# Kernel optimization log

Hardware: AMD Instinct MI355X
Metric: run time of the kernel (lower is better)

## Reference

```python
import jax, jax.numpy as jnp
import numpy as np

NUM_HEADS = 8
H_DIM = 24
COORDS_DIM = 3
NUM_W_PER_DIST = 8
BLOCK_SIZE = 128
N_HASHES = 3
N = 32768
HASH_DIM = H_DIM + (COORDS_DIM - 1) + 2  # q/k augmented with RPE coordinate terms


def layernorm(x, g, b, eps=1e-5):
    mu = x.mean(-1, keepdims=True)
    var = ((x - mu) ** 2).mean(-1, keepdims=True)
    return (x - mu) * jax.lax.rsqrt(var + eps) * g + b


def setup_inputs() -> dict:
    key = jax.random.key(0)
    ks = jax.random.split(key, 16)
    d, H = H_DIM, NUM_HEADS
    s = lambda i, shape, scale: jax.random.normal(ks[i], shape, jnp.float32) * scale
    return {
        "x": s(0, (N, d), 1.0),
        "coords": jax.random.uniform(ks[1], (N, COORDS_DIM), jnp.float32),
        "norm1_g": jnp.ones((d,), jnp.float32),
        "norm1_b": jnp.zeros((d,), jnp.float32),
        "Wq": s(2, (d, H * d), d ** -0.5),
        "Wk": s(3, (d, H * d), d ** -0.5),
        "Wv": s(4, (d, H * d), d ** -0.5),
        "w_rpe_W": s(5, (H * d, (COORDS_DIM - 1) * NUM_W_PER_DIST), 0.3),
        "Wo": s(6, (H * d, d), (H * d) ** -0.5),
        "bo": jnp.zeros((d,), jnp.float32),
        "norm2_g": jnp.ones((d,), jnp.float32),
        "norm2_b": jnp.zeros((d,), jnp.float32),
        "ff_W1": s(7, (d, d), d ** -0.5),
        "ff_b1": jnp.zeros((d,), jnp.float32),
        "ff_W2": s(8, (d, d), d ** -0.5),
        "ff_b2": jnp.zeros((d,), jnp.float32),
        "alphas": s(9, (N_HASHES, H, HASH_DIM), 1.0),  # E2LSH projection vectors
    }


def hept_attention(q, k, v, coords, w_rpe_W, alphas):
    # q,k,v: [n, H*d]. HEPT: fold RPE exp(-w*||dp||^2) into augmented q/k, then
    # n_hashes rounds of LSH sort + block-local attention, combined by softmax
    # over each round's log-normalizer (Reformer-style).
    n = q.shape[0]
    H, d, B = NUM_HEADS, H_DIM, BLOCK_SIZE
    nb = n // B
    q = q.reshape(n, H, d).transpose(1, 0, 2) * (d ** -0.5)  # [H,n,d]
    k = k.reshape(n, H, d).transpose(1, 0, 2)
    v = v.reshape(n, H, d).transpose(1, 0, 2)
    # per-head non-negative distance weights from w_rpe (mixture collapsed)
    Wm = w_rpe_W.reshape(H, d, COORDS_DIM - 1, NUM_W_PER_DIST)
    w = jnp.mean(Wm, axis=(1, 3)) ** 2                        # [H, c-1]
    p = coords[:, 1:]                                          # [n, c-1]
    sqn = jnp.einsum("hc,nc,nc->hn", w, p, p)                # w*||p||^2
    qp = jnp.sqrt(2.0) * jnp.sqrt(w)[:, None, :] * p[None]     # [H,n,c-1]
    ones = jnp.ones((H, n, 1), q.dtype)
    # q_hat.k_hat = q.k + 2*w*p_i.p_j - w|p_i|^2 - w|p_j|^2 = q.k - w*||p_i-p_j||^2
    q_hat = jnp.concatenate([q, qp, -sqn[..., None], ones], -1)  # [H,n,HASH_DIM]
    k_hat = jnp.concatenate([k, qp, ones, -sqn[..., None]], -1)
    outs, zs = [], []
    for r in range(N_HASHES):
        a = alphas[r]                                          # [H, HASH_DIM]
        iq = jnp.argsort(jnp.einsum("hne,he->hn", q_hat, a), -1)
        ik = jnp.argsort(jnp.einsum("hne,he->hn", k_hat, a), -1)
        qs = jnp.take_along_axis(q_hat, iq[..., None], 1).reshape(H, nb, B, -1)
        ks = jnp.take_along_axis(k_hat, ik[..., None], 1).reshape(H, nb, B, -1)
        vs = jnp.take_along_axis(v, ik[..., None], 1).reshape(H, nb, B, d)
        logits = jnp.einsum("hbqe,hbke->hbqk", qs, ks)         # [H,nb,B,B]
        z = jax.nn.logsumexp(logits, -1).reshape(H, n)
        o = jnp.einsum("hbqk,hbkd->hbqd", jax.nn.softmax(logits, -1), vs).reshape(H, n, d)
        inv = jnp.argsort(iq, -1)                              # unsort to input order
        outs.append(jnp.take_along_axis(o, inv[..., None], 1))
        zs.append(jnp.take_along_axis(z, inv, 1))
    wts = jax.nn.softmax(jnp.stack(zs), axis=0)[..., None]     # [R,H,n,1]
    out = (jnp.stack(outs) * wts).sum(0)                       # [H,n,d]
    return out.transpose(1, 0, 2).reshape(n, H * d)


def reference(x, coords, norm1_g, norm1_b, Wq, Wk, Wv, w_rpe_W, Wo, bo,
              norm2_g, norm2_b, ff_W1, ff_b1, ff_W2, ff_b2, alphas):
    xn = layernorm(x, norm1_g, norm1_b)
    q, k, v = xn @ Wq, xn @ Wk, xn @ Wv
    aggr = hept_attention(q, k, v, coords, w_rpe_W, alphas) @ Wo + bo
    x = x + aggr  # dropout is identity in eval mode
    h = layernorm(x, norm2_g, norm2_b)
    ff = jax.nn.relu(h @ ff_W1 + ff_b1) @ ff_W2 + ff_b2
    return x + ff
```

## Files before the change

kernel.cpp:

```cpp
#include <hip/hip_runtime.h>
#include <math.h>

#define NPT 32768
#define NH 8
#define HD 24
#define EDIM 28
#define NHASH 3
#define NSEG 48
#define NRH 24

typedef unsigned long long u64;
typedef unsigned short ushort;
typedef __attribute__((__vector_size__(8 * sizeof(short)))) short bf16x8;
typedef __attribute__((__vector_size__(4 * sizeof(float)))) float floatx4;

__device__ __forceinline__ ushort f2bf(float f) {
    unsigned u = __float_as_uint(f);
    unsigned r = u + 0x7FFF + ((u >> 16) & 1);
    return (ushort)(r >> 16);
}
__device__ __forceinline__ float us2f(ushort u) {
    return __uint_as_float(((unsigned)u) << 16);
}

__global__ __launch_bounds__(512) void k2s(
    const float* __restrict__ x, const float* __restrict__ n1g,
    const float* __restrict__ n1b, const float* __restrict__ coords,
    const float* __restrict__ wrpe, const float* __restrict__ Wq,
    const float* __restrict__ Wk, const float* __restrict__ alphas,
    u64* __restrict__ keys, float* __restrict__ xnf) {
    __shared__ double sA[2][24][NRH];
    __shared__ double sCt[NRH][4];
    __shared__ double sW64[16];
    __shared__ double sSc[16];
    __shared__ double sGB[48];
    __shared__ double sXn[8][24];
    int t = threadIdx.x;
    if (t < 16) {
        int h = t >> 1, c = t & 1;
        double s = 0.0;
        for (int i = 0; i < 24; i++)
            for (int j = 0; j < 8; j++)
                s += (double)wrpe[(h * 24 + i) * 16 + c * 8 + j];
        double m = s / 192.0;
        sW64[t] = m * m;
        sSc[t] = sqrt(2.0) * fabs(m);
    }
    if (t >= 64 && t < 88) {
        int tt = t - 64;
        sGB[tt] = (double)n1g[tt]; sGB[24 + tt] = (double)n1b[tt];
    }
    __syncthreads();
    const double QSCALE = 1.0 / sqrt(24.0);
    for (int idx = t; idx < 24 * NRH; idx += 512) {
        int i = idx / NRH, rh = idx % NRH;
        int h = rh & 7;
        double aq = 0.0, ak = 0.0;
        for (int e = 0; e < 24; e++) {
            double al = (double)alphas[rh * 28 + e];
            aq += (double)Wq[i * 192 + h * 24 + e] * al;
            ak += (double)Wk[i * 192 + h * 24 + e] * al;
        }
        sA[0][i][rh] = aq * QSCALE;
        sA[1][i][rh] = ak;
    }
    if (t < NRH) {
        int h = t & 7;
        sCt[t][0] = (double)alphas[t * 28 + 24] * sSc[h * 2 + 0];
        sCt[t][1] = (double)alphas[t * 28 + 25] * sSc[h * 2 + 1];
        sCt[t][2] = (double)alphas[t * 28 + 26];
        sCt[t][3] = (double)alphas[t * 28 + 27];
    }
    __syncthreads();
    int wv = t >> 6, l = t & 63;
    for (int g = 0; g < 8; g++) {
        int n = blockIdx.x * 64 + g * 8 + wv;
        double xv = (l < 24) ? (double)x[(u64)n * 24 + l] : 0.0;
        double s = xv;
        s += __shfl_xor(s, 1); s += __shfl_xor(s, 2); s += __shfl_xor(s, 4);
        s += __shfl_xor(s, 8); s += __shfl_xor(s, 16);
        double mu = s / 24.0;
        double d = (l < 24) ? (xv - mu) : 0.0;
        double v2 = d * d;
        v2 += __shfl_xor(v2, 1); v2 += __shfl_xor(v2, 2); v2 += __shfl_xor(v2, 4);
        v2 += __shfl_xor(v2, 8); v2 += __shfl_xor(v2, 16);
        double rstd = 1.0 / sqrt(v2 / 24.0 + 1e-5);
        if (l < 24) {
            double xn = d * rstd * sGB[l] + sGB[24 + l];
            sXn[wv][l] = xn;
            xnf[(u64)n * 24 + l] = (float)xn;
        }
        double p0 = (double)coords[(u64)n * 3 + 1];
        double p1 = (double)coords[(u64)n * 3 + 2];
        if (l < 2 * NRH) {
            int qk = l / NRH, rh = l % NRH;
            int h = rh & 7;
            double sqn = sW64[2 * h] * p0 * p0 + sW64[2 * h + 1] * p1 * p1;
            double acc = sCt[rh][0] * p0 + sCt[rh][1] * p1;
            acc += qk ? (sCt[rh][2] - sqn * sCt[rh][3]) : (sCt[rh][3] - sqn * sCt[rh][2]);
            for (int i = 0; i < 24; i++) acc += sXn[wv][i] * sA[qk][i][rh];
            u64 u = (u64)__double_as_longlong(acc);
            if (u >> 63) u = ~u; else u |= 0x8000000000000000ULL;
            u64 key = (u & ~(u64)32767) | (u64)n;
            keys[(u64)l * NPT + n] = key;
        }
    }
}

#define K2P_PTS 64
__global__ __launch_bounds__(640) void k2p(
    const float* __restrict__ xnf,
    const float* __restrict__ Wq, const float* __restrict__ Wk,
    const float* __restrict__ Wv, const float* __restrict__ coords,
    const float* __restrict__ wrpe,
    ushort* __restrict__ qhatB, ushort* __restrict__ khatB, ushort* __restrict__ varrB) {
    int t = threadIdx.x;
    int n0 = blockIdx.x * K2P_PTS;
    if (t < 576) {
        int m = t / 192, jj = t % 192;
        const float* W = (m == 0) ? Wq : ((m == 1) ? Wk : Wv);
        float wc[24];
#pragma unroll
        for (int i = 0; i < 24; i++) wc[i] = W[i * 192 + jj];
        const float scale = (m == 0) ? (float)(1.0 / sqrt(24.0)) : 1.0f;
        int h = jj / 24, e = jj % 24;
        ushort* outp = (m == 0) ? qhatB : ((m == 1) ? khatB : varrB);
        ushort* obase = outp + (u64)h * NPT * 32 + e;
        for (int p = 0; p < K2P_PTS; p++) {
            int n = n0 + p;
            const float* xr = xnf + (u64)n * 24;
            float acc = 0.f;
#pragma unroll
            for (int i = 0; i < 24; i++) acc += xr[i] * wc[i];
            obase[(u64)n * 32] = f2bf(acc * scale);
        }
    } else {
        int l = t - 576;
        int h2 = l >> 3, e2 = 24 + (l & 7);
        double m0 = 0.0, m1 = 0.0;
        for (int i = 0; i < 24; i++)
            for (int j = 0; j < 8; j++) {
                m0 += (double)wrpe[(h2 * 24 + i) * 16 + j];
                m1 += (double)wrpe[(h2 * 24 + i) * 16 + 8 + j];
            }
        m0 /= 192.0; m1 /= 192.0;
        double wa = m0 * m0, wb = m1 * m1;
        double c0 = sqrt(2.0) * fabs(m0), c1 = sqrt(2.0) * fabs(m1);
        ushort* qb = qhatB + (u64)h2 * NPT * 32 + e2;
        ushort* kb = khatB + (u64)h2 * NPT * 32 + e2;
        for (int p = 0; p < K2P_PTS; p++) {
            int n = n0 + p;
            double p0 = (double)coords[(u64)n * 3 + 1];
            double p1 = (double)coords[(u64)n * 3 + 2];
            float qv, kv;
            if (e2 < 26) {
                int c = e2 - 24;
                float qp = (float)((c ? c1 : c0) * (c ? p1 : p0));
                qv = qp; kv = qp;
            } else if (e2 < 28) {
                double sqn = wa * p0 * p0 + wb * p1 * p1;
                if (e2 == 26) { qv = (float)(-sqn); kv = 1.0f; }
                else          { qv = 1.0f; kv = (float)(-sqn); }
            } else {
                qv = 0.0f; kv = 0.0f;
            }
            qb[(u64)n * 32] = f2bf(qv);
            kb[(u64)n * 32] = f2bf(kv);
        }
    }
}

__device__ __forceinline__ u64 shflx64(u64 v, int d) {
    int lo = __shfl_xor((int)(unsigned)v, d);
    int hi = __shfl_xor((int)(unsigned)(v >> 32), d);
    return ((u64)(unsigned)hi << 32) | (unsigned)lo;
}
__device__ __forceinline__ void cswap(u64& a, u64& b, bool up) {
    if ((a > b) == up) { u64 tmp = a; a = b; b = tmp; }
}
__device__ __forceinline__ u64* sslot(u64* s, int i) {
    int a = i << 3;
    a ^= ((a >> 9) & 7) << 4;
    return (u64*)((char*)s + a);
}
__device__ __forceinline__ void reg_passes(u64 e[8], int ib, int K, int jmax) {
    for (int j = jmax; j >= 1; j >>= 1) {
#pragma unroll
        for (int k = 0; k < 8; k++)
            if ((k & j) == 0) cswap(e[k], e[k | j], ((ib + k) & K) == 0);
    }
}
__device__ __forceinline__ void shfl_passes(u64 e[8], int t, int segoff, int K, int jhi, int jlo) {
    for (int j = jhi; j >= jlo; j >>= 1) {
        int d = j >> 3;
        bool lower = (t & d) == 0;
        bool up = ((segoff + ((t & ~d) << 3)) & K) == 0;
        bool keepmin = (lower == up);
#pragma unroll
        for (int k = 0; k < 8; k++) {
            u64 o = shflx64(e[k], d);
            bool ownsm = e[k] < o;
            e[k] = (ownsm == keepmin) ? e[k] : o;
        }
    }
}

__global__ __launch_bounds__(1024) void sort_local_full(u64* keys) {
    __shared__ u64 s[8192];
    int t = threadIdx.x;
    u64 gbase = (u64)blockIdx.x * 8192;
    int segoff = (int)(gbase & 32767);
    int ib = segoff + t * 8;
    u64 e[8];
#pragma unroll
    for (int k = 0; k < 8; k++) e[k] = keys[gbase + t * 8 + k];
    reg_passes(e, ib, 2, 1);
    reg_passes(e, ib, 4, 2);
    reg_passes(e, ib, 8, 4);
    for (int K = 16; K <= 512; K <<= 1) {
        shfl_passes(e, t, segoff, K, K >> 1, 8);
        reg_passes(e, ib, K, 4);
    }
#pragma unroll
    for (int k = 0; k < 8; k++) *sslot(s, t * 8 + k) = e[k];
    __syncthreads();
    for (int K = 1024; K <= 8192; K <<= 1) {
        for (int j = K >> 1; j >= 512; j >>= 1) {
            for (int p = t; p < 4096; p += 1024) {
                int i = ((p & ~(j - 1)) << 1) | (p & (j - 1));
                int i2 = i | j;
                bool up = (((segoff + i) & K) == 0);
                u64 a = *sslot(s, i), b = *sslot(s, i2);
                if ((a > b) == up) { *sslot(s, i) = b; *sslot(s, i2) = a; }
            }
            __syncthreads();
        }
#pragma unroll
        for (int k = 0; k < 8; k++) e[k] = *sslot(s, t * 8 + k);
        shfl_passes(e, t, segoff, K, 256, 8);
        reg_passes(e, ib, K, 4);
        if (K < 8192) {
#pragma unroll
            for (int k = 0; k < 8; k++) *sslot(s, t * 8 + k) = e[k];
            __syncthreads();
        } else {
#pragma unroll
            for (int k = 0; k < 8; k++) keys[gbase + t * 8 + k] = e[k];
        }
    }
}

__global__ __launch_bounds__(1024) void sort_tail1_fused(
    const u64* __restrict__ kin, u64* __restrict__ kout) {
    __shared__ u64 s[8192];
    int t = threadIdx.x;
    u64 gbase = (u64)blockIdx.x * 8192;
    u64 pbase = gbase ^ 8192ULL;
    int ci = (int)((gbase >> 13) & 3);
    bool keepmin = (ci == 0) || (ci == 3);
    int segoff = (int)(gbase & 32767);
    int ib = segoff + t * 8;
    for (int i = t; i < 8192; i += 1024) {
        u64 a = kin[gbase + i];
        u64 b = kin[pbase + i];
        u64 mn = a < b ? a : b;
        u64 mx = a < b ? b : a;
        *sslot(s, i) = keepmin ? mn : mx;
    }
    __syncthreads();
    const int K = 16384;
    for (int j = 4096; j >= 512; j >>= 1) {
        for (int p = t; p < 4096; p += 1024) {
            int i = ((p & ~(j - 1)) << 1) | (p & (j - 1));
            int i2 = i | j;
            bool up = (((segoff + i) & K) == 0);
            u64 a = *sslot(s, i), b = *sslot(s, i2);
            if ((a > b) == up) { *sslot(s, i) = b; *sslot(s, i2) = a; }
        }
        __syncthreads();
    }
    u64 e[8];
#pragma unroll
    for (int k = 0; k < 8; k++) e[k] = *sslot(s, t * 8 + k);
    shfl_passes(e, t, segoff, K, 256, 8);
    reg_passes(e, ib, K, 4);
#pragma unroll
    for (int k = 0; k < 8; k++) kout[gbase + t * 8 + k] = e[k];
}

__global__ __launch_bounds__(1024) void sort_tail2_fused(
    const u64* __restrict__ kin, u64* __restrict__ kout) {
    __shared__ u64 s[8192];
    int t = threadIdx.x;
    u64 gbase = (u64)blockIdx.x * 8192;
    u64 segbase = gbase & ~(u64)32767;
    int ci = (int)((gbase >> 13) & 3);
    int segoff = (int)(gbase & 32767);
    for (int i = t; i < 8192; i += 1024) {
        u64 e0 = kin[segbase + i];
        u64 e1 = kin[segbase + 8192 + i];
        u64 e2 = kin[segbase + 16384 + i];
        u64 e3 = kin[segbase + 24576 + i];
        u64 m02 = e0 < e2 ? e0 : e2, M02 = e0 < e2 ? e2 : e0;
        u64 m13 = e1 < e3 ? e1 : e3, M13 = e1 < e3 ? e3 : e1;
        u64 r;
        if (ci == 0)      r = m02 < m13 ? m02 : m13;
        else if (ci == 1) r = m02 < m13 ? m13 : m02;
        else if (ci == 2) r = M02 < M13 ? M02 : M13;
        else              r = M02 < M13 ? M13 : M02;
        *sslot(s, i) = r;
    }
    __syncthreads();
    const int K = 32768;
    for (int j = 4096; j >= 512; j >>= 1) {
        for (int p = t; p < 4096; p += 1024) {
            int i = ((p & ~(j - 1)) << 1) | (p & (j - 1));
            int i2 = i | j;
            bool up = (((segoff + i) & K) == 0);
            u64 a = *sslot(s, i), b = *sslot(s, i2);
            if ((a > b) == up) { *sslot(s, i) = b; *sslot(s, i2) = a; }
        }
        __syncthreads();
    }
    u64 e[8];
#pragma unroll
    for (int k = 0; k < 8; k++) e[k] = *sslot(s, t * 8 + k);
    shfl_passes(e, t, segoff, K, 256, 128);
#pragma unroll
    for (int k = 0; k < 8; k++) kout[gbase + t * 8 + k] = e[k];
}

#define VT_STRIDE 136
#define P_STRIDE 72
__global__ __launch_bounds__(256, 4) void k3_attn(
    const u64* __restrict__ keys, const ushort* __restrict__ qhatB,
    const ushort* __restrict__ khatB, const ushort* __restrict__ varrB,
    ushort* __restrict__ ozB) {
    int rh3 = blockIdx.x % 24;
    int b = blockIdx.x / 24;
    int h = rh3 & 7, r = rh3 >> 3;
    __shared__ __align__(16) char smem[6528 + 18432 + 1024];
    short* sVt = (short*)smem;
    short* sP  = (short*)(smem + 6528);
    int* qidx  = (int*)(smem + 6528 + 18432);
    int* kidx  = qidx + 128;
    int t = threadIdx.x;
    int segQ = r * 8 + h, segK = 24 + r * 8 + h;
    if (t < 128) {
        qidx[t] = (int)(keys[(u64)segQ * NPT + b * 128 + t] & 32767ULL);
    } else {
        int i = t - 128;
        kidx[i] = (int)(keys[(u64)segK * NPT + b * 128 + i] & 32767ULL);
    }
    __syncthreads();

    int wave = t >> 6, L = t & 63;
    int quad = L >> 4, n16 = L & 15;

    const bf16x8* Qg = (const bf16x8*)(qhatB + (u64)h * NPT * 32);
    const bf16x8* Kg = (const bf16x8*)(khatB + (u64)h * NPT * 32);
    bf16x8 afr[2];
#pragma unroll
    for (int rtg = 0; rtg < 2; rtg++) {
        int qi = qidx[wave * 32 + rtg * 16 + n16];
        afr[rtg] = Qg[(u64)qi * 4 + quad];
    }
    bf16x8 bfr[8];
#pragma unroll
    for (int ct = 0; ct < 8; ct++) {
        int ki = kidx[ct * 16 + n16];
        bfr[ct] = Kg[(u64)ki * 4 + quad];
    }
    if (t < 128) {
        int ki = kidx[t];
        const bf16x8* vr = (const bf16x8*)(varrB + ((u64)h * NPT + ki) * 32);
        bf16x8 v0 = vr[0], v1 = vr[1], v2 = vr[2];
#pragma unroll
        for (int e = 0; e < 8; e++) {
            sVt[e * VT_STRIDE + t]        = v0[e];
            sVt[(8 + e) * VT_STRIDE + t]  = v1[e];
            sVt[(16 + e) * VT_STRIDE + t] = v2[e];
        }
    }
    __syncthreads();

    floatx4 acc[2][8];
#pragma unroll
    for (int rtg = 0; rtg < 2; rtg++)
#pragma unroll
        for (int ct = 0; ct < 8; ct++)
            acc[rtg][ct] = (floatx4){0.f, 0.f, 0.f, 0.f};
#pragma unroll
    for (int ct = 0; ct < 8; ct++) {
#pragma unroll
        for (int rtg = 0; rtg < 2; rtg++)
            acc[rtg][ct] = __builtin_amdgcn_mfma_f32_16x16x32_bf16(afr[rtg], bfr[ct], acc[rtg][ct], 0, 0, 0);
    }

    float mrow[2][4], srow[2][4];
#pragma unroll
    for (int rtg = 0; rtg < 2; rtg++) {
#pragma unroll
        for (int rg = 0; rg < 4; rg++) {
            float m = -1e30f;
#pragma unroll
            for (int ct = 0; ct < 8; ct++) m = fmaxf(m, acc[rtg][ct][rg]);
            m = fmaxf(m, __shfl_xor(m, 1));
            m = fmaxf(m, __shfl_xor(m, 2));
            m = fmaxf(m, __shfl_xor(m, 4));
            m = fmaxf(m, __shfl_xor(m, 8));
            mrow[rtg][rg] = m;
            float s = 0.0f;
            int row = wave * 32 + rtg * 16 + quad * 4 + rg;
#pragma unroll
            for (int ct = 0; ct < 8; ct++) {
                float p = __expf(acc[rtg][ct][rg] - m);
                s += p;
                if (ct < 4) sP[row * P_STRIDE + ct * 16 + n16] = (short)f2bf(p);
            }
            s += __shfl_xor(s, 1);
            s += __shfl_xor(s, 2);
            s += __shfl_xor(s, 4);
            s += __shfl_xor(s, 8);
            srow[rtg][rg] = s;
        }
    }

    floatx4 occ[2][2];
#pragma unroll
    for (int rtg = 0; rtg < 2; rtg++)
#pragma unroll
        for (int ct2 = 0; ct2 < 2; ct2++)
            occ[rtg][ct2] = (floatx4){0.f, 0.f, 0.f, 0.f};
#pragma unroll
    for (int ks = 0; ks < 2; ks++) {
        bf16x8 bv[2], av[2];
#pragma unroll
        for (int ct2 = 0; ct2 < 2; ct2++)
            bv[ct2] = *(const bf16x8*)(sVt + (ct2 * 16 + n16) * VT_STRIDE + ks * 32 + quad * 8);
#pragma unroll
        for (int rtg = 0; rtg < 2; rtg++)
            av[rtg] = *(const bf16x8*)(sP + (wave * 32 + rtg * 16 + n16) * P_STRIDE + ks * 32 + quad * 8);
#pragma unroll
        for (int rtg = 0; rtg < 2; rtg++)
#pragma unroll
            for (int ct2 = 0; ct2 < 2; ct2++)
                occ[rtg][ct2] = __builtin_amdgcn_mfma_f32_16x16x32_bf16(av[rtg], bv[ct2], occ[rtg][ct2], 0, 0, 0);
    }
#pragma unroll
    for (int rtg = 0; rtg < 2; rtg++) {
#pragma unroll
        for (int rg = 0; rg < 4; rg++) {
            int row = wave * 32 + rtg * 16 + quad * 4 + rg;
#pragma unroll
            for (int ct = 4; ct < 8; ct++) {
                float p = __expf(acc[rtg][ct][rg] - mrow[rtg][rg]);
                sP[row * P_STRIDE + (ct - 4) * 16 + n16] = (short)f2bf(p);
            }
        }
    }
#pragma unroll
    for (int ks = 2; ks < 4; ks++) {
        bf16x8 bv[2], av[2];
#pragma unroll
        for (int ct2 = 0; ct2 < 2; ct2++)
            bv[ct2] = *(const bf16x8*)(sVt + (ct2 * 16 + n16) * VT_STRIDE + ks * 32 + quad * 8);
#pragma unroll
        for (int rtg = 0; rtg < 2; rtg++)
            av[rtg] = *(const bf16x8*)(sP + (wave * 32 + rtg * 16 + n16) * P_STRIDE + (ks - 2) * 32 + quad * 8);
#pragma unroll
        for (int rtg = 0; rtg < 2; rtg++)
#pragma unroll
            for (int ct2 = 0; ct2 < 2; ct2++)
                occ[rtg][ct2] = __builtin_amdgcn_mfma_f32_16x16x32_bf16(av[rtg], bv[ct2], occ[rtg][ct2], 0, 0, 0);
    }

#pragma unroll
    for (int rtg = 0; rtg < 2; rtg++) {
#pragma unroll
        for (int rg = 0; rg < 4; rg++) {
            int row = wave * 32 + rtg * 16 + quad * 4 + rg;
            int oi = qidx[row];
            float inv = 1.0f / srow[rtg][rg];
            ushort* orow = ozB + ((u64)segQ * NPT + oi) * 32;
#pragma unroll
            for (int ct2 = 0; ct2 < 2; ct2++) {
                int col = ct2 * 16 + n16;
                if (col < 24) orow[col] = f2bf(occ[rtg][ct2][rg] * inv);
            }
            if (n16 == 0)
                *(float*)(orow + 24) = mrow[rtg][rg] + __logf(srow[rtg][rg]);
        }
    }
}

#define K4PTS 32
#define AT_STR 196
#define W_STR 28
__global__ __launch_bounds__(256) void k4_final(
    const ushort* __restrict__ ozB,
    const float* __restrict__ x,
    const float* __restrict__ Wo, const float* __restrict__ bo,
    const float* __restrict__ g2, const float* __restrict__ b2,
    const float* __restrict__ W1, const float* __restrict__ b1f,
    const float* __restrict__ W2, const float* __restrict__ b2f,
    float* __restrict__ out) {
    __shared__ __align__(16) float sWoT[24][AT_STR];
    __shared__ __align__(16) float sW1T[24][W_STR], sW2T[24][W_STR];
    __shared__ float sB[5 * 24];
    __shared__ __align__(16) float attn[K4PTS][AT_STR];
    __shared__ float xrow[K4PTS][25];
    __shared__ __align__(16) float h2row[K4PTS][W_STR];
    __shared__ __align__(16) float ffrow[K4PTS][W_STR];
    int t = threadIdx.x;
    int base = blockIdx.x * K4PTS;
    for (int i = t; i < 4608; i += 256) sWoT[i % 24][i / 24] = Wo[i];
    for (int i = t; i < 576; i += 256) {
        sW1T[i % 24][i / 24] = W1[i];
        sW2T[i % 24][i / 24] = W2[i];
    }
    if (t < 24) {
        sB[t] = bo[t]; sB[24 + t] = g2[t]; sB[48 + t] = b2[t];
        sB[72 + t] = b1f[t]; sB[96 + t] = b2f[t];
    }
    if (t < K4PTS * 4) {
        int p = t >> 2, c = 24 + (t & 3);
        h2row[p][c] = 0.f; ffrow[p][c] = 0.f;
    }
    if (t < 24 * 4) {
        int rr = t >> 2, c = 24 + (t & 3);
        sW1T[rr][c] = 0.f; sW2T[rr][c] = 0.f;
    }
    {
        int p = t >> 3, h = t & 7;
        int n = base + p;
        const ushort* r0 = ozB + ((u64)(0 * 8 + h) * NPT + n) * 32;
        const ushort* r1 = ozB + ((u64)(1 * 8 + h) * NPT + n) * 32;
        const ushort* r2 = ozB + ((u64)(2 * 8 + h) * NPT + n) * 32;
        float z0 = *(const float*)(r0 + 24);
        float z1 = *(const float*)(r1 + 24);
        float z2 = *(const float*)(r2 + 24);
        float zm = fmaxf(z0, fmaxf(z1, z2));
        float e0 = __expf(z0 - zm), e1 = __expf(z1 - zm), e2 = __expf(z2 - zm);
        float inv = 1.0f / (e0 + e1 + e2);
        float w0 = e0 * inv, w1 = e1 * inv, w2 = e2 * inv;
#pragma unroll
        for (int e = 0; e < 24; e++)
            attn[p][h * 24 + e] = w0 * us2f(r0[e]) + w1 * us2f(r1[e]) + w2 * us2f(r2[e]);
    }
    __syncthreads();
    int p = t >> 3, oe = t & 7;
    int n = base + p;
    {
        const floatx4* ap = (const floatx4*)&attn[p][0];
        const floatx4* w0p = (const floatx4*)&sWoT[oe][0];
        const floatx4* w1p = (const floatx4*)&sWoT[oe + 8][0];
        const floatx4* w2p = (const floatx4*)&sWoT[oe + 16][0];
        floatx4 A0 = {0.f, 0.f, 0.f, 0.f}, A1 = A0, A2 = A0;
        for (int ii = 0; ii < 48; ii++) {
            floatx4 av = ap[ii];
            A0 += av * w0p[ii];
            A1 += av * w1p[ii];
            A2 += av * w2p[ii];
        }
        float a0 = A0[0] + A0[1] + A0[2] + A0[3];
        float a1 = A1[0] + A1[1] + A1[2] + A1[3];
        float a2 = A2[0] + A2[1] + A2[2] + A2[3];
        xrow[p][oe]      = x[n * 24 + oe]      + a0 + sB[oe];
        xrow[p][oe + 8]  = x[n * 24 + oe + 8]  + a1 + sB[oe + 8];
        xrow[p][oe + 16] = x[n * 24 + oe + 16] + a2 + sB[oe + 16];
    }
    float mu, rstd;
    {
        float s = xrow[p][oe] + xrow[p][oe + 8] + xrow[p][oe + 16];
        s += __shfl_xor(s, 1); s += __shfl_xor(s, 2); s += __shfl_xor(s, 4);
        mu = s / 24.0f;
        float v0 = xrow[p][oe] - mu, v1 = xrow[p][oe + 8] - mu, v2 = xrow[p][oe + 16] - mu;
        float v = v0 * v0 + v1 * v1 + v2 * v2;
        v += __shfl_xor(v, 1); v += __shfl_xor(v, 2); v += __shfl_xor(v, 4);
        rstd = 1.0f / sqrtf(v / 24.0f + 1e-5f);
    }
    h2row[p][oe]      = (xrow[p][oe] - mu)      * rstd * sB[24 + oe]      + sB[48 + oe];
    h2row[p][oe + 8]  = (xrow[p][oe + 8] - mu)  * rstd * sB[24 + oe + 8]  + sB[48 + oe + 8];
    h2row[p][oe + 16] = (xrow[p][oe + 16] - mu) * rstd * sB[24 + oe + 16] + sB[48 + oe + 16];
    {
        const floatx4* hp = (const floatx4*)&h2row[p][0];
        const floatx4* w0p = (const floatx4*)&sW1T[oe][0];
        const floatx4* w1p = (const floatx4*)&sW1T[oe + 8][0];
        const floatx4* w2p = (const floatx4*)&sW1T[oe + 16][0];
        floatx4 A0 = {0.f, 0.f, 0.f, 0.f}, A1 = A0, A2 = A0;
#pragma unroll
        for (int ii = 0; ii < 6; ii++) {
            floatx4 hv = hp[ii];
            A0 += hv * w0p[ii];
            A1 += hv * w1p[ii];
            A2 += hv * w2p[ii];
        }
        ffrow[p][oe]      = fmaxf(A0[0]+A0[1]+A0[2]+A0[3] + sB[72 + oe], 0.f);
        ffrow[p][oe + 8]  = fmaxf(A1[0]+A1[1]+A1[2]+A1[3] + sB[72 + oe + 8], 0.f);
        ffrow[p][oe + 16] = fmaxf(A2[0]+A2[1]+A2[2]+A2[3] + sB[72 + oe + 16], 0.f);
    }
    {
        const floatx4* fp = (const floatx4*)&ffrow[p][0];
        const floatx4* w0p = (const floatx4*)&sW2T[oe][0];
        const floatx4* w1p = (const floatx4*)&sW2T[oe + 8][0];
        const floatx4* w2p = (const floatx4*)&sW2T[oe + 16][0];
        floatx4 A0 = {0.f, 0.f, 0.f, 0.f}, A1 = A0, A2 = A0;
#pragma unroll
        for (int ii = 0; ii < 6; ii++) {
            floatx4 fv = fp[ii];
            A0 += fv * w0p[ii];
            A1 += fv * w1p[ii];
            A2 += fv * w2p[ii];
        }
        out[n * 24 + oe]      = xrow[p][oe]      + A0[0]+A0[1]+A0[2]+A0[3] + sB[96 + oe];
        out[n * 24 + oe + 8]  = xrow[p][oe + 8]  + A1[0]+A1[1]+A1[2]+A1[3] + sB[96 + oe + 8];
        out[n * 24 + oe + 16] = xrow[p][oe + 16] + A2[0]+A2[1]+A2[2]+A2[3] + sB[96 + oe + 16];
    }
}

extern "C" void kernel_launch(void* const* d_in, const int* in_sizes, int n_in,
                              void* d_out, int out_size, void* d_ws, size_t ws_size,
                              hipStream_t stream) {
    const float* x      = (const float*)d_in[0];
    const float* coords = (const float*)d_in[1];
    const float* n1g    = (const float*)d_in[2];
    const float* n1b    = (const float*)d_in[3];
    const float* Wq     = (const float*)d_in[4];
    const float* Wk     = (const float*)d_in[5];
    const float* Wv     = (const float*)d_in[6];
    const float* wrpe   = (const float*)d_in[7];
    const float* Wo     = (const float*)d_in[8];
    const float* bo     = (const float*)d_in[9];
    const float* n2g    = (const float*)d_in[10];
    const float* n2b    = (const float*)d_in[11];
    const float* W1     = (const float*)d_in[12];
    const float* b1     = (const float*)d_in[13];
    const float* W2     = (const float*)d_in[14];
    const float* b2     = (const float*)d_in[15];
    const float* alphas = (const float*)d_in[16];

    char* ws = (char*)d_ws;
    size_t off = 0;
    auto alloc = [&](size_t bytes) -> void* {
        void* p = ws + off;
        off = (off + bytes + 255) & ~(size_t)255;
        return p;
    };
    float*  xnf   = (float*)alloc((size_t)NPT * 24 * 4);
    ushort* qhatB = (ushort*)alloc((size_t)NH * NPT * 32 * 2);
    ushort* khatB = (ushort*)alloc((size_t)NH * NPT * 32 * 2);
    ushort* varrB = (ushort*)alloc((size_t)NH * NPT * 32 * 2);
    u64*    keys  = (u64*)alloc((size_t)NSEG * NPT * 8);
    u64*    keys2 = (u64*)alloc((size_t)NSEG * NPT * 8);
    ushort* ozB   = (ushort*)alloc((size_t)NHASH * NH * NPT * 32 * 2);
    if (off > ws_size) return;

    k2s<<<NPT / 64, 512, 0, stream>>>(x, n1g, n1b, coords, wrpe, Wq, Wk, alphas,
                                      keys, xnf);
    k2p<<<NPT / K2P_PTS, 640, 0, stream>>>(xnf, Wq, Wk, Wv, coords, wrpe,
                                           qhatB, khatB, varrB);
    sort_local_full<<<192, 1024, 0, stream>>>(keys);
    sort_tail1_fused<<<192, 1024, 0, stream>>>(keys, keys2);
    sort_tail2_fused<<<192, 1024, 0, stream>>>(keys2, keys);
    k3_attn<<<256 * 8 * 3, 256, 0, stream>>>(keys, qhatB, khatB, varrB, ozB);
    k4_final<<<NPT / K4PTS, 256, 0, stream>>>(ozB, x, Wo, bo, n2g, n2b,
                                              W1, b1, W2, b2, (float*)d_out);
}
```

Before: 307.9 us.

## Fuse hash-key and projection kernels; merge sort passes into one cooperative kernel

Merges the hash-key/layernorm kernel with the bf16 q/k/v projection kernel, so each block reuses its layernorm output and the shared RPE weights instead of recomputing them from global memory. The three bitonic sort kernels become one cooperative launch that uses grid-wide syncs between merge stages and keeps each thread's keys in registers, which avoids separate launches and some global reloads. Risks: the xnf values read back within the same block depend on global memory visibility after __syncthreads, and a cooperative launch with 192 blocks of 1024 threads must fit co-resident on the device.

```diff
diff --git a/kernel.cpp b/kernel.cpp
--- a/kernel.cpp
+++ b/kernel.cpp
@@ -1,5 +1,8 @@
 #include <hip/hip_runtime.h>
+#include <hip/hip_cooperative_groups.h>
 #include <math.h>
+
+namespace cg = cooperative_groups;
 
 #define NPT 32768
 #define NH 8
@@ -23,12 +26,14 @@
     return __uint_as_float(((unsigned)u) << 16);
 }
 
-__global__ __launch_bounds__(512) void k2s(
+__global__ __launch_bounds__(640) void k2sp(
     const float* __restrict__ x, const float* __restrict__ n1g,
     const float* __restrict__ n1b, const float* __restrict__ coords,
     const float* __restrict__ wrpe, const float* __restrict__ Wq,
-    const float* __restrict__ Wk, const float* __restrict__ alphas,
-    u64* __restrict__ keys, float* __restrict__ xnf) {
+    const float* __restrict__ Wk, const float* __restrict__ Wv,
+    const float* __restrict__ alphas,
+    u64* __restrict__ keys, float* __restrict__ xnf,
+    ushort* __restrict__ qhatB, ushort* __restrict__ khatB, ushort* __restrict__ varrB) {
     __shared__ double sA[2][24][NRH];
     __shared__ double sCt[NRH][4];
     __shared__ double sW64[16];
@@ -52,7 +57,7 @@
     }
     __syncthreads();
     const double QSCALE = 1.0 / sqrt(24.0);
-    for (int idx = t; idx < 24 * NRH; idx += 512) {
+    for (int idx = t; idx < 24 * NRH; idx += 640) {
         int i = idx / NRH, rh = idx % NRH;
         int h = rh & 7;
         double aq = 0.0, ak = 0.0;
@@ -72,50 +77,43 @@
         sCt[t][3] = (double)alphas[t * 28 + 27];
     }
     __syncthreads();
-    int wv = t >> 6, l = t & 63;
-    for (int g = 0; g < 8; g++) {
-        int n = blockIdx.x * 64 + g * 8 + wv;
-        double xv = (l < 24) ? (double)x[(u64)n * 24 + l] : 0.0;
-        double s = xv;
-        s += __shfl_xor(s, 1); s += __shfl_xor(s, 2); s += __shfl_xor(s, 4);
-        s += __shfl_xor(s, 8); s += __shfl_xor(s, 16);
-        double mu = s / 24.0;
-        double d = (l < 24) ? (xv - mu) : 0.0;
-        double v2 = d * d;
-        v2 += __shfl_xor(v2, 1); v2 += __shfl_xor(v2, 2); v2 += __shfl_xor(v2, 4);
-        v2 += __shfl_xor(v2, 8); v2 += __shfl_xor(v2, 16);
-        double rstd = 1.0 / sqrt(v2 / 24.0 + 1e-5);
-        if (l < 24) {
-            double xn = d * rstd * sGB[l] + sGB[24 + l];
-            sXn[wv][l] = xn;
-            xnf[(u64)n * 24 + l] = (float)xn;
-        }
-        double p0 = (double)coords[(u64)n * 3 + 1];
-        double p1 = (double)coords[(u64)n * 3 + 2];
-        if (l < 2 * NRH) {
-            int qk = l / NRH, rh = l % NRH;
-            int h = rh & 7;
-            double sqn = sW64[2 * h] * p0 * p0 + sW64[2 * h + 1] * p1 * p1;
-            double acc = sCt[rh][0] * p0 + sCt[rh][1] * p1;
-            acc += qk ? (sCt[rh][2] - sqn * sCt[rh][3]) : (sCt[rh][3] - sqn * sCt[rh][2]);
-            for (int i = 0; i < 24; i++) acc += sXn[wv][i] * sA[qk][i][rh];
-            u64 u = (u64)__double_as_longlong(acc);
-            if (u >> 63) u = ~u; else u |= 0x8000000000000000ULL;
-            u64 key = (u & ~(u64)32767) | (u64)n;
-            keys[(u64)l * NPT + n] = key;
-        }
-    }
-}
-
-#define K2P_PTS 64
-__global__ __launch_bounds__(640) void k2p(
-    const float* __restrict__ xnf,
-    const float* __restrict__ Wq, const float* __restrict__ Wk,
-    const float* __restrict__ Wv, const float* __restrict__ coords,
-    const float* __restrict__ wrpe,
-    ushort* __restrict__ qhatB, ushort* __restrict__ khatB, ushort* __restrict__ varrB) {
-    int t = threadIdx.x;
-    int n0 = blockIdx.x * K2P_PTS;
+    if (t < 512) {
+        int wv = t >> 6, l = t & 63;
+        for (int g = 0; g < 8; g++) {
+            int n = blockIdx.x * 64 + g * 8 + wv;
+            double xv = (l < 24) ? (double)x[(u64)n * 24 + l] : 0.0;
+            double s = xv;
+            s += __shfl_xor(s, 1); s += __shfl_xor(s, 2); s += __shfl_xor(s, 4);
+            s += __shfl_xor(s, 8); s += __shfl_xor(s, 16);
+            double mu = s / 24.0;
+            double d = (l < 24) ? (xv - mu) : 0.0;
+            double v2 = d * d;
+            v2 += __shfl_xor(v2, 1); v2 += __shfl_xor(v2, 2); v2 += __shfl_xor(v2, 4);
+            v2 += __shfl_xor(v2, 8); v2 += __shfl_xor(v2, 16);
+            double rstd = 1.0 / sqrt(v2 / 24.0 + 1e-5);
+            if (l < 24) {
+                double xn = d * rstd * sGB[l] + sGB[24 + l];
+                sXn[wv][l] = xn;
+                xnf[(u64)n * 24 + l] = (float)xn;
+            }
+            double p0 = (double)coords[(u64)n * 3 + 1];
+            double p1 = (double)coords[(u64)n * 3 + 2];
+            if (l < 2 * NRH) {
+                int qk = l / NRH, rh = l % NRH;
+                int h = rh & 7;
+                double sqn = sW64[2 * h] * p0 * p0 + sW64[2 * h + 1] * p1 * p1;
+                double acc = sCt[rh][0] * p0 + sCt[rh][1] * p1;
+                acc += qk ? (sCt[rh][2] - sqn * sCt[rh][3]) : (sCt[rh][3] - sqn * sCt[rh][2]);
+                for (int i = 0; i < 24; i++) acc += sXn[wv][i] * sA[qk][i][rh];
+                u64 u = (u64)__double_as_longlong(acc);
+                if (u >> 63) u = ~u; else u |= 0x8000000000000000ULL;
+                u64 key = (u & ~(u64)32767) | (u64)n;
+                keys[(u64)l * NPT + n] = key;
+            }
+        }
+    }
+    __syncthreads();
+    int n0 = blockIdx.x * 64;
     if (t < 576) {
         int m = t / 192, jj = t % 192;
         const float* W = (m == 0) ? Wq : ((m == 1) ? Wk : Wv);
@@ -126,7 +124,7 @@
         int h = jj / 24, e = jj % 24;
         ushort* outp = (m == 0) ? qhatB : ((m == 1) ? khatB : varrB);
         ushort* obase = outp + (u64)h * NPT * 32 + e;
-        for (int p = 0; p < K2P_PTS; p++) {
+        for (int p = 0; p < 64; p++) {
             int n = n0 + p;
             const float* xr = xnf + (u64)n * 24;
             float acc = 0.f;
@@ -137,18 +135,11 @@
     } else {
         int l = t - 576;
         int h2 = l >> 3, e2 = 24 + (l & 7);
-        double m0 = 0.0, m1 = 0.0;
-        for (int i = 0; i < 24; i++)
-            for (int j = 0; j < 8; j++) {
-                m0 += (double)wrpe[(h2 * 24 + i) * 16 + j];
-                m1 += (double)wrpe[(h2 * 24 + i) * 16 + 8 + j];
-            }
-        m0 /= 192.0; m1 /= 192.0;
-        double wa = m0 * m0, wb = m1 * m1;
-        double c0 = sqrt(2.0) * fabs(m0), c1 = sqrt(2.0) * fabs(m1);
+        double wa = sW64[h2 * 2], wb = sW64[h2 * 2 + 1];
+        double c0 = sSc[h2 * 2], c1 = sSc[h2 * 2 + 1];
         ushort* qb = qhatB + (u64)h2 * NPT * 32 + e2;
         ushort* kb = khatB + (u64)h2 * NPT * 32 + e2;
-        for (int p = 0; p < K2P_PTS; p++) {
+        for (int p = 0; p < 64; p++) {
             int n = n0 + p;
             double p0 = (double)coords[(u64)n * 3 + 1];
             double p1 = (double)coords[(u64)n * 3 + 2];
@@ -205,11 +196,12 @@
     }
 }
 
-__global__ __launch_bounds__(1024) void sort_local_full(u64* keys) {
+__global__ __launch_bounds__(1024) void sort_coop(u64* keys, u64* keys2) {
     __shared__ u64 s[8192];
     int t = threadIdx.x;
     u64 gbase = (u64)blockIdx.x * 8192;
     int segoff = (int)(gbase & 32767);
+    int ci = (int)((gbase >> 13) & 3);
     int ib = segoff + t * 8;
     u64 e[8];
 #pragma unroll
@@ -248,86 +240,75 @@
             for (int k = 0; k < 8; k++) keys[gbase + t * 8 + k] = e[k];
         }
     }
-}
-
-__global__ __launch_bounds__(1024) void sort_tail1_fused(
-    const u64* __restrict__ kin, u64* __restrict__ kout) {
-    __shared__ u64 s[8192];
-    int t = threadIdx.x;
-    u64 gbase = (u64)blockIdx.x * 8192;
-    u64 pbase = gbase ^ 8192ULL;
-    int ci = (int)((gbase >> 13) & 3);
-    bool keepmin = (ci == 0) || (ci == 3);
-    int segoff = (int)(gbase & 32767);
-    int ib = segoff + t * 8;
-    for (int i = t; i < 8192; i += 1024) {
-        u64 a = kin[gbase + i];
-        u64 b = kin[pbase + i];
-        u64 mn = a < b ? a : b;
-        u64 mx = a < b ? b : a;
-        *sslot(s, i) = keepmin ? mn : mx;
-    }
-    __syncthreads();
-    const int K = 16384;
-    for (int j = 4096; j >= 512; j >>= 1) {
-        for (int p = t; p < 4096; p += 1024) {
-            int i = ((p & ~(j - 1)) << 1) | (p & (j - 1));
-            int i2 = i | j;
-            bool up = (((segoff + i) & K) == 0);
-            u64 a = *sslot(s, i), b = *sslot(s, i2);
-            if ((a > b) == up) { *sslot(s, i) = b; *sslot(s, i2) = a; }
-        }
+    cg::this_grid().sync();
+    {
+        u64 pbase = gbase ^ 8192ULL;
+        bool keepmin = (ci == 0) || (ci == 3);
+#pragma unroll
+        for (int k = 0; k < 8; k++) {
+            u64 b = keys[pbase + t * 8 + k];
+            u64 mn = e[k] < b ? e[k] : b;
+            u64 mx = e[k] < b ? b : e[k];
+            e[k] = keepmin ? mn : mx;
+        }
+#pragma unroll
+        for (int k = 0; k < 8; k++) *sslot(s, t * 8 + k) = e[k];
         __syncthreads();
-    }
-    u64 e[8];
-#pragma unroll
-    for (int k = 0; k < 8; k++) e[k] = *sslot(s, t * 8 + k);
-    shfl_passes(e, t, segoff, K, 256, 8);
-    reg_passes(e, ib, K, 4);
-#pragma unroll
-    for (int k = 0; k < 8; k++) kout[gbase + t * 8 + k] = e[k];
-}
-
-__global__ __launch_bounds__(1024) void sort_tail2_fused(
-    const u64* __restrict__ kin, u64* __restrict__ kout) {
-    __shared__ u64 s[8192];
-    int t = threadIdx.x;
-    u64 gbase = (u64)blockIdx.x * 8192;
-    u64 segbase = gbase & ~(u64)32767;
-    int ci = (int)((gbase >> 13) & 3);
-    int segoff = (int)(gbase & 32767);
-    for (int i = t; i < 8192; i += 1024) {
-        u64 e0 = kin[segbase + i];
-        u64 e1 = kin[segbase + 8192 + i];
-        u64 e2 = kin[segbase + 16384 + i];
-        u64 e3 = kin[segbase + 24576 + i];
-        u64 m02 = e0 < e2 ? e0 : e2, M02 = e0 < e2 ? e2 : e0;
-        u64 m13 = e1 < e3 ? e1 : e3, M13 = e1 < e3 ? e3 : e1;
-        u64 r;
-        if (ci == 0)      r = m02 < m13 ? m02 : m13;
-        else if (ci == 1) r = m02 < m13 ? m13 : m02;
-        else if (ci == 2) r = M02 < M13 ? M02 : M13;
-        else              r = M02 < M13 ? M13 : M02;
-        *sslot(s, i) = r;
-    }
-    __syncthreads();
-    const int K = 32768;
-    for (int j = 4096; j >= 512; j >>= 1) {
-        for (int p = t; p < 4096; p += 1024) {
-            int i = ((p & ~(j - 1)) << 1) | (p & (j - 1));
-            int i2 = i | j;
-            bool up = (((segoff + i) & K) == 0);
-            u64 a = *sslot(s, i), b = *sslot(s, i2);
-            if ((a > b) == up) { *sslot(s, i) = b; *sslot(s, i2) = a; }
+        const int K = 16384;
+        for (int j = 4096; j >= 512; j >>= 1) {
+            for (int p = t; p < 4096; p += 1024) {
+                int i = ((p & ~(j - 1)) << 1) | (p & (j - 1));
+                int i2 = i | j;
+                bool up = (((segoff + i) & K) == 0);
+                u64 a = *sslot(s, i), b = *sslot(s, i2);
+                if ((a > b) == up) { *sslot(s, i) = b; *sslot(s, i2) = a; }
+            }
+            __syncthreads();
+        }
+#pragma unroll
+        for (int k = 0; k < 8; k++) e[k] = *sslot(s, t * 8 + k);
+        shfl_passes(e, t, segoff, K, 256, 8);
+        reg_passes(e, ib, K, 4);
+#pragma unroll
+        for (int k = 0; k < 8; k++) keys2[gbase + t * 8 + k] = e[k];
+    }
+    cg::this_grid().sync();
+    {
+        u64 segbase = gbase & ~(u64)32767;
+#pragma unroll
+        for (int k = 0; k < 8; k++) {
+            int i = t * 8 + k;
+            u64 v0 = (ci == 0) ? e[k] : keys2[segbase + i];
+            u64 v1 = (ci == 1) ? e[k] : keys2[segbase + 8192 + i];
+            u64 v2 = (ci == 2) ? e[k] : keys2[segbase + 16384 + i];
+            u64 v3 = (ci == 3) ? e[k] : keys2[segbase + 24576 + i];
+            u64 m02 = v0 < v2 ? v0 : v2, M02 = v0 < v2 ? v2 : v0;
+            u64 m13 = v1 < v3 ? v1 : v3, M13 = v1 < v3 ? v3 : v1;
+            u64 r;
+            if (ci == 0)      r = m02 < m13 ? m02 : m13;
+            else if (ci == 1) r = m02 < m13 ? m13 : m02;
+            else if (ci == 2) r = M02 < M13 ? M02 : M13;
+            else              r = M02 < M13 ? M13 : M02;
+            *sslot(s, i) = r;
         }
         __syncthreads();
-    }
-    u64 e[8];
-#pragma unroll
-    for (int k = 0; k < 8; k++) e[k] = *sslot(s, t * 8 + k);
-    shfl_passes(e, t, segoff, K, 256, 128);
-#pragma unroll
-    for (int k = 0; k < 8; k++) kout[gbase + t * 8 + k] = e[k];
+        const int K = 32768;
+        for (int j = 4096; j >= 512; j >>= 1) {
+            for (int p = t; p < 4096; p += 1024) {
+                int i = ((p & ~(j - 1)) << 1) | (p & (j - 1));
+                int i2 = i | j;
+                bool up = (((segoff + i) & K) == 0);
+                u64 a = *sslot(s, i), b = *sslot(s, i2);
+                if ((a > b) == up) { *sslot(s, i) = b; *sslot(s, i2) = a; }
+            }
+            __syncthreads();
+        }
+#pragma unroll
+        for (int k = 0; k < 8; k++) e[k] = *sslot(s, t * 8 + k);
+        shfl_passes(e, t, segoff, K, 256, 128);
+#pragma unroll
+        for (int k = 0; k < 8; k++) keys[gbase + t * 8 + k] = e[k];
+    }
 }
 
 #define VT_STRIDE 136
@@ -656,13 +637,13 @@
     ushort* ozB   = (ushort*)alloc((size_t)NHASH * NH * NPT * 32 * 2);
     if (off > ws_size) return;
 
-    k2s<<<NPT / 64, 512, 0, stream>>>(x, n1g, n1b, coords, wrpe, Wq, Wk, alphas,
-                                      keys, xnf);
-    k2p<<<NPT / K2P_PTS, 640, 0, stream>>>(xnf, Wq, Wk, Wv, coords, wrpe,
-                                           qhatB, khatB, varrB);
-    sort_local_full<<<192, 1024, 0, stream>>>(keys);
-    sort_tail1_fused<<<192, 1024, 0, stream>>>(keys, keys2);
-    sort_tail2_fused<<<192, 1024, 0, stream>>>(keys2, keys);
+    k2sp<<<NPT / 64, 640, 0, stream>>>(x, n1g, n1b, coords, wrpe, Wq, Wk, Wv,
+                                       alphas, keys, xnf, qhatB, khatB, varrB);
+    {
+        void* sargs[] = { (void*)&keys, (void*)&keys2 };
+        hipLaunchCooperativeKernel((const void*)sort_coop, dim3(192), dim3(1024),
+                                   sargs, 0, stream);
+    }
     k3_attn<<<256 * 8 * 3, 256, 0, stream>>>(keys, qhatB, khatB, varrB, ozB);
     k4_final<<<NPT / K4PTS, 256, 0, stream>>>(ozB, x, Wo, bo, n2g, n2b,
                                               W1, b1, W2, b2, (float*)d_out);
```

Result: slower. 440.3 us (+43.0%).
